# Kernel optimization log

Hardware: AMD Instinct MI355X
Metric: run time of the kernel (lower is better)

The kernel has to match this reference:

```python
import jax, jax.numpy as jnp
import numpy as np

IN_CH = 256
OUT_CH = 128
N = 6144
ADJ_P = 0.01  # edge density -> avg degree ~61


def setup_inputs() -> dict:
    key = jax.random.key(0)
    ks = jax.random.split(key, 8)
    x = jax.random.normal(ks[0], (1, IN_CH, N), dtype=jnp.float32)
    adj = (jax.random.uniform(ks[1], (N, N)) < ADJ_P).astype(jnp.float32)
    W_fts = jax.random.normal(ks[2], (OUT_CH, IN_CH), dtype=jnp.float32) * 0.05
    w1 = jax.random.normal(ks[3], (OUT_CH,), dtype=jnp.float32) * 0.05
    b1 = jnp.zeros((1,), dtype=jnp.float32)
    w2 = jax.random.normal(ks[4], (OUT_CH,), dtype=jnp.float32) * 0.05
    b2 = jnp.zeros((1,), dtype=jnp.float32)
    vars_bias = jax.random.normal(ks[5], (1, N, OUT_CH), dtype=jnp.float32) * 0.02
    return {"x": x, "adj": adj, "W_fts": W_fts, "w1": w1, "b1": b1,
            "w2": w2, "b2": b2, "vars_bias": vars_bias}


def reference(x, adj, W_fts, w1, b1, w2, b2, vars_bias):
    # fts = Conv1d(in, out, k=1, bias=False)(x): [1, OUT_CH, N]
    fts = jnp.einsum('oi,bin->bon', W_fts, x)
    f = fts[0]  # [OUT_CH, N]
    # f1/f2 = Conv1d(out, 1, 1)(fts) -> per-node scalars [N]
    f1 = jnp.einsum('o,on->n', w1, f) + b1  # [N]
    f2 = jnp.einsum('o,on->n', w2, f) + b2  # [N]
    # scores[i,j] = leaky_relu(adj[i,j]*f1[i] + adj[i,j]*f2[j], 0.2)
    scores = jax.nn.leaky_relu(adj * f1[:, None] + adj * f2[None, :], 0.2)
    # sparse_softmax2d: per-row softmax masked to nonzero entries
    mask = (scores != 0).astype(scores.dtype)
    m = jnp.max(scores, axis=1, keepdims=True)  # stabilizer; cancels in ratio
    exps = jnp.exp(scores - m) * mask
    coefs = exps / jnp.sum(exps, axis=1, keepdims=True)  # [N, N]
    # vals = coefs @ fts.T : [N, OUT_CH]
    vals = coefs @ f.T
    # add bias, permute to [1, OUT_CH, N]
    ret = jnp.transpose(vals[None, :, :] + vars_bias, (0, 2, 1))
    return ret
```

## Files before the change

### kernel.cpp

```cpp
#include <hip/hip_runtime.h>

#define NN  6144
#define ICH 256
#define OCH 128
#define QW  160

typedef float vf4 __attribute__((ext_vector_type(4)));

__global__ __launch_bounds__(256) void k_fts(const float* __restrict__ x,
        const float* __restrict__ W, const float* __restrict__ w1,
        const float* __restrict__ w2, float* __restrict__ ft,
        float* __restrict__ f1, float* __restrict__ f2) {
    __shared__ float xs[32][32];
    __shared__ float Ws[32][OCH + 4];
    const int n0  = blockIdx.x * 32;
    const int tid = threadIdx.x;
    const int oq = (tid & 31) * 4;
    const int nq = (tid >> 5) * 4;
    float acc[4][4] = {};
    for (int k0 = 0; k0 < ICH; k0 += 32) {
        __syncthreads();
        {
            const int nn = tid & 31;
            const int kb = tid >> 5;
#pragma unroll
            for (int r = 0; r < 4; ++r)
                xs[kb + r * 8][nn] = x[(size_t)(k0 + kb + r * 8) * NN + n0 + nn];
        }
        {
            const int kk = tid & 31;
            const int ob = tid >> 5;
#pragma unroll
            for (int r = 0; r < 16; ++r) {
                const int o = ob + r * 8;
                Ws[kk][o] = W[o * ICH + k0 + kk];
            }
        }
        __syncthreads();
#pragma unroll
        for (int kk = 0; kk < 32; ++kk) {
            const float4 xv = *(const float4*)&xs[kk][nq];
            const float4 wv = *(const float4*)&Ws[kk][oq];
            const float xa[4] = {xv.x, xv.y, xv.z, xv.w};
            const float wa[4] = {wv.x, wv.y, wv.z, wv.w};
#pragma unroll
            for (int a = 0; a < 4; ++a)
#pragma unroll
                for (int b = 0; b < 4; ++b)
                    acc[a][b] = fmaf(xa[a], wa[b], acc[a][b]);
        }
    }
#pragma unroll
    for (int a = 0; a < 4; ++a) {
        float4 v = make_float4(acc[a][0], acc[a][1], acc[a][2], acc[a][3]);
        *(float4*)&ft[(size_t)(n0 + nq + a) * OCH + oq] = v;
    }
    const float4 w1v = *(const float4*)(w1 + oq);
    const float4 w2v = *(const float4*)(w2 + oq);
    float p1[4], p2[4];
#pragma unroll
    for (int a = 0; a < 4; ++a) {
        p1[a] = acc[a][0] * w1v.x + acc[a][1] * w1v.y + acc[a][2] * w1v.z + acc[a][3] * w1v.w;
        p2[a] = acc[a][0] * w2v.x + acc[a][1] * w2v.y + acc[a][2] * w2v.z + acc[a][3] * w2v.w;
    }
#pragma unroll
    for (int m = 16; m > 0; m >>= 1) {
#pragma unroll
        for (int a = 0; a < 4; ++a) {
            p1[a] += __shfl_xor(p1[a], m);
            p2[a] += __shfl_xor(p2[a], m);
        }
    }
    if ((tid & 31) == 0) {
#pragma unroll
        for (int a = 0; a < 4; ++a) {
            f1[n0 + nq + a] = p1[a];
            f2[n0 + nq + a] = p2[a];
        }
    }
}

__global__ __launch_bounds__(256) void k_mask(const float* __restrict__ adj,
        unsigned* __restrict__ mask) {
    const int lane = threadIdx.x & 63;
    const int wave = threadIdx.x >> 6;
    const int u = blockIdx.x * 4 + wave;
    const int i = u / 3;
    const int g = u - i * 3;
    const float* p = adj + (size_t)i * NN + g * 2048 + lane * 4;
    vf4 a[8];
#pragma unroll
    for (int k = 0; k < 8; ++k)
        a[k] = *(const vf4*)(p + k * 256);
    unsigned w = 0;
#pragma unroll
    for (int k = 0; k < 8; ++k) {
        w |= (a[k].x != 0.f ? 1u : 0u) << (4 * k);
        w |= (a[k].y != 0.f ? 2u : 0u) << (4 * k);
        w |= (a[k].z != 0.f ? 4u : 0u) << (4 * k);
        w |= (a[k].w != 0.f ? 8u : 0u) << (4 * k);
    }
    mask[(size_t)(i * 3 + g) * 64 + lane] = w;
}

__global__ __launch_bounds__(256) void k_edge(const unsigned* __restrict__ mask,
        const float* __restrict__ ft, const float* __restrict__ f1,
        const float* __restrict__ f2, const float* __restrict__ b1,
        const float* __restrict__ b2, const float* __restrict__ vb,
        float* __restrict__ out) {
    __shared__ float2 q[4][QW];
    const int tid  = threadIdx.x;
    const int lane = tid & 63;
    const int wave = tid >> 6;
    const int i = blockIdx.x * 4 + wave;
    const float s1 = f1[i] + b1[0] + b2[0];
    unsigned mw[3];
#pragma unroll
    for (int g = 0; g < 3; ++g)
        mw[g] = mask[(size_t)(i * 3 + g) * 64 + lane];
    const unsigned long long lt = (1ull << lane) - 1;
    float den = 0.f;
    int cnt = 0;
#pragma unroll
    for (int g = 0; g < 3; ++g) {
        unsigned w = mw[g];
        for (;;) {
            const unsigned long long act = __ballot(w != 0);
            if (!act) break;
            if (w) {
                const int b = __builtin_ctz(w);
                w &= w - 1;
                const int j = g * 2048 + (b >> 2) * 256 + lane * 4 + (b & 3);
                float s = s1 + f2[j];
                s = s > 0.f ? s : 0.2f * s;
                const float e = __expf(s);
                den += e;
                const int slot = cnt + (int)__popcll(act & lt);
                if (slot < QW)
                    q[wave][slot] = make_float2(__int_as_float(j), e);
            }
            cnt += (int)__popcll(act);
        }
    }
#pragma unroll
    for (int off = 32; off > 0; off >>= 1) den += __shfl_xor(den, off);
    const float inv = 1.f / den;
    const int nE = cnt < QW ? cnt : QW;
    const int half = lane >> 5;
    const int c0 = (lane & 31) * 4;
    float4 nm = make_float4(0.f, 0.f, 0.f, 0.f);
#pragma unroll 4
    for (int idx = half; idx < nE; idx += 2) {
        const float2 pe = q[wave][idx];
        const int   j = __float_as_int(pe.x);
        const float e = pe.y;
        const float4 g4 = *(const float4*)(ft + (size_t)j * OCH + c0);
        nm.x = fmaf(e, g4.x, nm.x);
        nm.y = fmaf(e, g4.y, nm.y);
        nm.z = fmaf(e, g4.z, nm.z);
        nm.w = fmaf(e, g4.w, nm.w);
    }
    nm.x += __shfl_xor(nm.x, 32);
    nm.y += __shfl_xor(nm.y, 32);
    nm.z += __shfl_xor(nm.z, 32);
    nm.w += __shfl_xor(nm.w, 32);
    if (half == 0) {
        const float4 bv = *(const float4*)(vb + (size_t)i * OCH + c0);
        out[(size_t)(c0    ) * NN + i] = fmaf(nm.x, inv, bv.x);
        out[(size_t)(c0 + 1) * NN + i] = fmaf(nm.y, inv, bv.y);
        out[(size_t)(c0 + 2) * NN + i] = fmaf(nm.z, inv, bv.z);
        out[(size_t)(c0 + 3) * NN + i] = fmaf(nm.w, inv, bv.w);
    }
}

extern "C" void kernel_launch(void* const* d_in, const int* in_sizes, int n_in,
                              void* d_out, int out_size, void* d_ws, size_t ws_size,
                              hipStream_t stream) {
    const float* x   = (const float*)d_in[0];
    const float* adj = (const float*)d_in[1];
    const float* W   = (const float*)d_in[2];
    const float* w1  = (const float*)d_in[3];
    const float* b1  = (const float*)d_in[4];
    const float* w2  = (const float*)d_in[5];
    const float* b2  = (const float*)d_in[6];
    const float* vb  = (const float*)d_in[7];
    float* out = (float*)d_out;

    char* ws = (char*)d_ws;
    float*    ft   = (float*)ws;
    float*    f1   = (float*)(ws + 3145728);
    float*    f2   = (float*)(ws + 3145728 + 24576);
    unsigned* mask = (unsigned*)(ws + 3194880);

    k_fts<<<dim3(NN / 32), 256, 0, stream>>>(x, W, w1, w2, ft, f1, f2);
    k_mask<<<dim3(NN * 3 / 4), 256, 0, stream>>>(adj, mask);
    k_edge<<<dim3(NN / 4), 256, 0, stream>>>(mask, ft, f1, f2, b1, b2, vb, out);
}
```

Baseline: 274.8 us.

## Fuse adjacency mask build into edge kernel via direct global-to-LDS row loads

New measurement: 279.8 us. About the same (+1.8%).

```diff
diff --git a/kernel.cpp b/kernel.cpp
--- a/kernel.cpp
+++ b/kernel.cpp
@@ -80,50 +80,42 @@
     }
 }
 
-__global__ __launch_bounds__(256) void k_mask(const float* __restrict__ adj,
-        unsigned* __restrict__ mask) {
-    const int lane = threadIdx.x & 63;
-    const int wave = threadIdx.x >> 6;
-    const int u = blockIdx.x * 4 + wave;
-    const int i = u / 3;
-    const int g = u - i * 3;
-    const float* p = adj + (size_t)i * NN + g * 2048 + lane * 4;
-    vf4 a[8];
-#pragma unroll
-    for (int k = 0; k < 8; ++k)
-        a[k] = *(const vf4*)(p + k * 256);
-    unsigned w = 0;
-#pragma unroll
-    for (int k = 0; k < 8; ++k) {
-        w |= (a[k].x != 0.f ? 1u : 0u) << (4 * k);
-        w |= (a[k].y != 0.f ? 2u : 0u) << (4 * k);
-        w |= (a[k].z != 0.f ? 4u : 0u) << (4 * k);
-        w |= (a[k].w != 0.f ? 8u : 0u) << (4 * k);
-    }
-    mask[(size_t)(i * 3 + g) * 64 + lane] = w;
-}
-
-__global__ __launch_bounds__(256) void k_edge(const unsigned* __restrict__ mask,
+__global__ __launch_bounds__(128) void k_row(const float* __restrict__ adj,
         const float* __restrict__ ft, const float* __restrict__ f1,
         const float* __restrict__ f2, const float* __restrict__ b1,
         const float* __restrict__ b2, const float* __restrict__ vb,
         float* __restrict__ out) {
-    __shared__ float2 q[4][QW];
+    __shared__ float  rowbuf[2][NN];
+    __shared__ float2 q[2][QW];
     const int tid  = threadIdx.x;
     const int lane = tid & 63;
     const int wave = tid >> 6;
-    const int i = blockIdx.x * 4 + wave;
+    const int i = blockIdx.x * 2 + wave;
+    const float* arow = adj + (size_t)i * NN;
+#pragma unroll
+    for (int w = 0; w < 24; ++w) {
+        __builtin_amdgcn_global_load_lds(
+            (const __attribute__((address_space(1))) void*)(arow + w * 256 + lane * 4),
+            (__attribute__((address_space(3))) void*)(&rowbuf[wave][w * 256]),
+            16, 0, 0);
+    }
     const float s1 = f1[i] + b1[0] + b2[0];
-    unsigned mw[3];
-#pragma unroll
-    for (int g = 0; g < 3; ++g)
-        mw[g] = mask[(size_t)(i * 3 + g) * 64 + lane];
+    __syncthreads();
     const unsigned long long lt = (1ull << lane) - 1;
+    float2* qw = q[wave];
     float den = 0.f;
     int cnt = 0;
 #pragma unroll
     for (int g = 0; g < 3; ++g) {
-        unsigned w = mw[g];
+        unsigned w = 0;
+#pragma unroll
+        for (int k = 0; k < 8; ++k) {
+            const vf4 a4 = *(const vf4*)&rowbuf[wave][g * 2048 + k * 256 + lane * 4];
+            w |= (a4.x != 0.f ? 1u : 0u) << (4 * k);
+            w |= (a4.y != 0.f ? 2u : 0u) << (4 * k);
+            w |= (a4.z != 0.f ? 4u : 0u) << (4 * k);
+            w |= (a4.w != 0.f ? 8u : 0u) << (4 * k);
+        }
         for (;;) {
             const unsigned long long act = __ballot(w != 0);
             if (!act) break;
@@ -137,7 +129,7 @@
                 den += e;
                 const int slot = cnt + (int)__popcll(act & lt);
                 if (slot < QW)
-                    q[wave][slot] = make_float2(__int_as_float(j), e);
+                    qw[slot] = make_float2(__int_as_float(j), e);
             }
             cnt += (int)__popcll(act);
         }
@@ -151,7 +143,7 @@
     float4 nm = make_float4(0.f, 0.f, 0.f, 0.f);
 #pragma unroll 4
     for (int idx = half; idx < nE; idx += 2) {
-        const float2 pe = q[wave][idx];
+        const float2 pe = qw[idx];
         const int   j = __float_as_int(pe.x);
         const float e = pe.y;
         const float4 g4 = *(const float4*)(ft + (size_t)j * OCH + c0);
@@ -187,12 +179,10 @@
     float* out = (float*)d_out;
 
     char* ws = (char*)d_ws;
-    float*    ft   = (float*)ws;
-    float*    f1   = (float*)(ws + 3145728);
-    float*    f2   = (float*)(ws + 3145728 + 24576);
-    unsigned* mask = (unsigned*)(ws + 3194880);
+    float* ft = (float*)ws;
+    float* f1 = (float*)(ws + 3145728);
+    float* f2 = (float*)(ws + 3145728 + 24576);
 
     k_fts<<<dim3(NN / 32), 256, 0, stream>>>(x, W, w1, w2, ft, f1, f2);
-    k_mask<<<dim3(NN * 3 / 4), 256, 0, stream>>>(adj, mask);
-    k_edge<<<dim3(NN / 4), 256, 0, stream>>>(mask, ft, f1, f2, b1, b2, vb, out);
+    k_row<<<dim3(NN / 2), 128, 0, stream>>>(adj, ft, f1, f2, b1, b2, vb, out);
 }
```

## Make mask kernel persistent with double-buffered adjacency loads and XCD-aware mapping

Applied to the files above, without the earlier changes.

After: 272.2 us. Within noise of the previous version (-1.0%).

```diff
diff --git a/kernel.cpp b/kernel.cpp
--- a/kernel.cpp
+++ b/kernel.cpp
@@ -80,27 +80,39 @@
     }
 }
 
-__global__ __launch_bounds__(256) void k_mask(const float* __restrict__ adj,
+__global__ __launch_bounds__(256) void k_mask_ps(const float* __restrict__ adj,
         unsigned* __restrict__ mask) {
     const int lane = threadIdx.x & 63;
     const int wave = threadIdx.x >> 6;
-    const int u = blockIdx.x * 4 + wave;
-    const int i = u / 3;
-    const int g = u - i * 3;
-    const float* p = adj + (size_t)i * NN + g * 2048 + lane * 4;
-    vf4 a[8];
+    const int r = blockIdx.x & 7;
+    const int s = blockIdx.x >> 3;
+    const int q = s * 4 + wave;
+    int c = r * 2304 + q;
+    const float* base0 = adj + (size_t)c * 2048 + lane * 4;
+    vf4 buf[2][8];
 #pragma unroll
     for (int k = 0; k < 8; ++k)
-        a[k] = *(const vf4*)(p + k * 256);
-    unsigned w = 0;
-#pragma unroll
-    for (int k = 0; k < 8; ++k) {
-        w |= (a[k].x != 0.f ? 1u : 0u) << (4 * k);
-        w |= (a[k].y != 0.f ? 2u : 0u) << (4 * k);
-        w |= (a[k].z != 0.f ? 4u : 0u) << (4 * k);
-        w |= (a[k].w != 0.f ? 8u : 0u) << (4 * k);
-    }
-    mask[(size_t)(i * 3 + g) * 64 + lane] = w;
+        buf[0][k] = *(const vf4*)(base0 + k * 256);
+#pragma unroll
+    for (int t = 0; t < 9; ++t) {
+        if (t < 8) {
+            const float* pn = adj + ((size_t)c + 256) * 2048 + lane * 4;
+#pragma unroll
+            for (int k = 0; k < 8; ++k)
+                buf[(t + 1) & 1][k] = *(const vf4*)(pn + k * 256);
+        }
+        unsigned w = 0;
+#pragma unroll
+        for (int k = 0; k < 8; ++k) {
+            const vf4 a4 = buf[t & 1][k];
+            w |= (a4.x != 0.f ? 1u : 0u) << (4 * k);
+            w |= (a4.y != 0.f ? 2u : 0u) << (4 * k);
+            w |= (a4.z != 0.f ? 4u : 0u) << (4 * k);
+            w |= (a4.w != 0.f ? 8u : 0u) << (4 * k);
+        }
+        mask[(size_t)c * 64 + lane] = w;
+        c += 256;
+    }
 }
 
 __global__ __launch_bounds__(256) void k_edge(const unsigned* __restrict__ mask,
@@ -112,7 +124,7 @@
     const int tid  = threadIdx.x;
     const int lane = tid & 63;
     const int wave = tid >> 6;
-    const int i = blockIdx.x * 4 + wave;
+    const int i = (blockIdx.x & 7) * 768 + (blockIdx.x >> 3) * 4 + wave;
     const float s1 = f1[i] + b1[0] + b2[0];
     unsigned mw[3];
 #pragma unroll
@@ -193,6 +205,6 @@
     unsigned* mask = (unsigned*)(ws + 3194880);
 
     k_fts<<<dim3(NN / 32), 256, 0, stream>>>(x, W, w1, w2, ft, f1, f2);
-    k_mask<<<dim3(NN * 3 / 4), 256, 0, stream>>>(adj, mask);
+    k_mask_ps<<<dim3(512), 256, 0, stream>>>(adj, mask);
     k_edge<<<dim3(NN / 4), 256, 0, stream>>>(mask, ft, f1, f2, b1, b2, vb, out);
 }
```
